# Kernel tuning notes

Measured on AMD Instinct MI355X. Metric: run time of the kernel, lower is better.

Reference implementation:

```python
import jax, jax.numpy as jnp
import numpy as np

SEQ, D = 4096, 1024  # vector_size == dimension == 1024


def setup_inputs() -> dict:
    key = jax.random.key(0)
    ks = jax.random.split(key, 7)
    s = 1.0 / np.sqrt(D)
    return {
        "X": jax.random.normal(ks[0], (SEQ, D), dtype=jnp.float32),
        "Wq": jax.random.normal(ks[1], (D, D), dtype=jnp.float32) * s,
        "bq": jax.random.normal(ks[2], (D,), dtype=jnp.float32) * s,
        "Wk": jax.random.normal(ks[3], (D, D), dtype=jnp.float32) * s,
        "bk": jax.random.normal(ks[4], (D,), dtype=jnp.float32) * s,
        "Wv": jax.random.normal(ks[5], (D, D), dtype=jnp.float32) * s,
        "bv": jax.random.normal(ks[6], (D,), dtype=jnp.float32) * s,
    }


def reference(X, Wq, bq, Wk, bk, Wv, bv):
    # Batched QKV projections (nn.Linear: x @ W^T + b), replacing the per-vector loop.
    Q = X @ Wq.T + bq            # [S, D]
    K = X @ Wk.T + bk            # [S, D]
    V = X @ Wv.T + bv            # [S, D]
    scale = 1.0 / jnp.sqrt(jnp.asarray(D, dtype=X.dtype))
    scores = (Q @ K.T) * scale   # [S, S]
    attn = jax.nn.softmax(scores, axis=1)
    return attn @ V              # [S, D]
```

## Files before the change

kernel.cpp:

```cpp
#include <hip/hip_runtime.h>
#include <hip/hip_bf16.h>
#include <stdint.h>


typedef __bf16 bf16_t;
typedef __bf16 bf16x4 __attribute__((ext_vector_type(4)));
typedef __bf16 bf16x8 __attribute__((ext_vector_type(8)));
typedef float f32x4 __attribute__((ext_vector_type(4)));

#define AS1 __attribute__((address_space(1)))
#define AS3 __attribute__((address_space(3)))

__device__ __forceinline__ void async_ld16(const void* g, void* l) {
  __builtin_amdgcn_global_load_lds((AS1 void*)g, (AS3 void*)l, 16, 0, 0);
}

template <int MODE, int BN, int BK>
__global__ __launch_bounds__(256, 2) void gemm_k(
    const bf16_t* __restrict__ A, const bf16_t* __restrict__ B, const int ld,
    const int Klen,
    bf16_t* __restrict__ o0, bf16_t* __restrict__ o1, bf16_t* __restrict__ o2,
    const float* __restrict__ b0, const float* __restrict__ b1,
    const float* __restrict__ b2, float* __restrict__ fout,
    float* __restrict__ rowsum) {
  constexpr int NF = BN / 32;
  constexpr int KS = BK / 32;
  constexpr int CH = BK / 8;
  constexpr int RS = 256 / CH;
  __shared__ bf16_t As[128 * BK];
  __shared__ bf16_t Bs[BN * BK];

  const int t = threadIdx.x;
  const int lane = t & 63;
  const int wave = t >> 6;
  const int wm = wave >> 1;
  const int wn = wave & 1;
  const int q = lane >> 4;
  const int l16 = lane & 15;
  const int wnoff = wn * (BN / 2);

  int m0, n0;
  if constexpr (MODE == 1) {
    const int bid = blockIdx.y * 32 + blockIdx.x;
    const int xcd = bid & 7, sl = bid >> 3;
    m0 = ((xcd >> 2) * 16 + (sl >> 3)) * 128;
    n0 = ((xcd & 3) * 8 + (sl & 7)) * BN;
  } else {
    n0 = blockIdx.x * BN;
    m0 = blockIdx.y * 128;
  }
  const int k0 = blockIdx.z * Klen;

  const f32x4 zero4 = {0.f, 0.f, 0.f, 0.f};
  f32x4 acc[4][NF];
#pragma unroll
  for (int i = 0; i < 4; ++i)
#pragma unroll
    for (int j = 0; j < NF; ++j) acc[i][j] = zero4;

  const int srow = t / CH;
  const int schunk =
      (t % CH) ^ ((BK == 32) ? ((srow >> 1) & 3) : (srow & 7));
  const bf16_t* Ab = A + (size_t)(m0 + srow) * ld + k0 + schunk * 8;
  const bf16_t* Bb = B + (size_t)(n0 + srow) * ld + k0 + schunk * 8;
  bf16_t* Asl = As + t * 8;
  bf16_t* Bsl = Bs + t * 8;

  const int xf = (BK == 32) ? ((l16 >> 1) & 3) : (l16 & 7);
  const int ar = wm * 64 + l16;
  const int br = wnoff + l16;

  for (int kt = 0; kt < Klen; kt += BK) {
#pragma unroll
    for (int rr = 0; rr < 128 / RS; ++rr)
      async_ld16(Ab + kt + (size_t)(rr * RS) * ld, Asl + rr * RS * BK);
#pragma unroll
    for (int rr = 0; rr < BN / RS; ++rr)
      async_ld16(Bb + kt + (size_t)(rr * RS) * ld, Bsl + rr * RS * BK);
    __syncthreads();

#pragma unroll
    for (int s = 0; s < KS; ++s) {
      bf16x8 fa[4], fb[NF];
#pragma unroll
      for (int im = 0; im < 4; ++im)
        fa[im] = *(const bf16x8*)(As + (ar + im * 16) * BK +
                                  (((s * 4 + q) ^ xf) * 8));
#pragma unroll
      for (int j = 0; j < NF; ++j)
        fb[j] = *(const bf16x8*)(Bs + (br + j * 16) * BK +
                                 (((s * 4 + q) ^ xf) * 8));
#pragma unroll
      for (int im = 0; im < 4; ++im)
#pragma unroll
        for (int j = 0; j < NF; ++j)
          acc[im][j] = __builtin_amdgcn_mfma_f32_16x16x32_bf16(
              fa[im], fb[j], acc[im][j], 0, 0, 0);
    }
    __syncthreads();
  }

  const int mBase = m0 + wm * 64 + q * 4;

  if constexpr (MODE == 0) {
    const int sel = n0 >> 10;
    const int nl0 = (n0 & 1023) + wnoff + l16;
    const float* bias = (sel == 0) ? b0 : ((sel == 1) ? b1 : b2);
    const float sc = (sel == 0) ? 0.03125f : 1.0f;
#pragma unroll
    for (int j = 0; j < NF; ++j) {
      const int nl = nl0 + j * 16;
      const float bb = bias[nl];
#pragma unroll
      for (int im = 0; im < 4; ++im) {
        const int mr = mBase + im * 16;
        if (sel < 2) {
          bf16_t* dst = (sel == 0) ? o0 : o1;
#pragma unroll
          for (int r = 0; r < 4; ++r)
            dst[(size_t)(mr + r) * 1024 + nl] =
                (bf16_t)((acc[im][j][r] + bb) * sc);
        } else {
          bf16x4 v;
#pragma unroll
          for (int r = 0; r < 4; ++r) v[r] = (bf16_t)(acc[im][j][r] + bb);
          *(bf16x4*)(o2 + (size_t)nl * 4096 + mr) = v;
        }
      }
    }
  } else if constexpr (MODE == 1) {
    float ps[4][4];
#pragma unroll
    for (int im = 0; im < 4; ++im)
#pragma unroll
      for (int r = 0; r < 4; ++r) ps[im][r] = 0.f;
#pragma unroll
    for (int j = 0; j < NF; ++j) {
      const int n = n0 + wnoff + j * 16 + l16;
#pragma unroll
      for (int im = 0; im < 4; ++im) {
        const int mr = mBase + im * 16;
#pragma unroll
        for (int r = 0; r < 4; ++r) {
          const float e = __expf(acc[im][j][r]);
          ps[im][r] += e;
          o0[(size_t)(mr + r) * 4096 + n] = (bf16_t)e;
        }
      }
    }
#pragma unroll
    for (int im = 0; im < 4; ++im)
#pragma unroll
      for (int r = 0; r < 4; ++r) {
        float v = ps[im][r];
        v += __shfl_xor(v, 1);
        v += __shfl_xor(v, 2);
        v += __shfl_xor(v, 4);
        v += __shfl_xor(v, 8);
        ps[im][r] = v;
      }
    if (l16 == 0) {
#pragma unroll
      for (int im = 0; im < 4; ++im)
#pragma unroll
        for (int r = 0; r < 4; ++r)
          atomicAdd(rowsum + mBase + im * 16 + r, ps[im][r]);
    }
  } else {
    const int z = blockIdx.z;
    float inv[4][4];
#pragma unroll
    for (int im = 0; im < 4; ++im)
#pragma unroll
      for (int r = 0; r < 4; ++r)
        inv[im][r] = 1.0f / rowsum[mBase + im * 16 + r];
    if (z < 3) {
      bf16_t* pp = (z == 0) ? o0 : ((z == 1) ? o1 : o2);
#pragma unroll
      for (int im = 0; im < 4; ++im) {
        const int mr = mBase + im * 16;
#pragma unroll
        for (int j = 0; j < NF; ++j) {
          const int n = n0 + wnoff + j * 16 + l16;
#pragma unroll
          for (int r = 0; r < 4; ++r)
            pp[(size_t)(mr + r) * 1024 + n] =
                (bf16_t)(acc[im][j][r] * inv[im][r]);
        }
      }
    } else {
#pragma unroll
      for (int im = 0; im < 4; ++im) {
        const int mr = mBase + im * 16;
#pragma unroll
        for (int j = 0; j < NF; ++j) {
          const int n = n0 + wnoff + j * 16 + l16;
#pragma unroll
          for (int r = 0; r < 4; ++r)
            fout[(size_t)(mr + r) * 1024 + n] = acc[im][j][r] * inv[im][r];
        }
      }
    }
  }
}

__global__ __launch_bounds__(256) void cvt_all(
    const float* __restrict__ X, const float* __restrict__ Wq,
    const float* __restrict__ Wk, const float* __restrict__ Wv,
    bf16_t* __restrict__ Xb, bf16_t* __restrict__ Wb,
    float* __restrict__ rowsum) {
  int i = blockIdx.x * 256 + threadIdx.x;
  if (i >= 1835008) {
    rowsum[i - 1835008] = 0.f;
    return;
  }
  const float* src;
  bf16_t* dst;
  int off;
  if (i < 1048576) {
    src = X; dst = Xb; off = i;
  } else {
    const int w = i - 1048576;
    const int sel = w >> 18;
    off = w & 0x3FFFF;
    src = (sel == 0) ? Wq : ((sel == 1) ? Wk : Wv);
    dst = Wb + (size_t)sel * (1024 * 1024);
  }
  const float4 v = ((const float4*)src)[off];
  bf16x4 o;
  o[0] = (bf16_t)v.x; o[1] = (bf16_t)v.y; o[2] = (bf16_t)v.z; o[3] = (bf16_t)v.w;
  ((bf16x4*)dst)[off] = o;
}

__global__ __launch_bounds__(256) void reduce_out(
    const bf16_t* __restrict__ p0, const bf16_t* __restrict__ p1,
    const bf16_t* __restrict__ p2, float* __restrict__ out) {
  const int i = blockIdx.x * 256 + threadIdx.x;
  const bf16x8 a = ((const bf16x8*)p0)[i];
  const bf16x8 b = ((const bf16x8*)p1)[i];
  const bf16x8 c = ((const bf16x8*)p2)[i];
  float4 lo = ((const float4*)out)[2 * i];
  float4 hi = ((const float4*)out)[2 * i + 1];
  lo.x += (float)a[0] + (float)b[0] + (float)c[0];
  lo.y += (float)a[1] + (float)b[1] + (float)c[1];
  lo.z += (float)a[2] + (float)b[2] + (float)c[2];
  lo.w += (float)a[3] + (float)b[3] + (float)c[3];
  hi.x += (float)a[4] + (float)b[4] + (float)c[4];
  hi.y += (float)a[5] + (float)b[5] + (float)c[5];
  hi.z += (float)a[6] + (float)b[6] + (float)c[6];
  hi.w += (float)a[7] + (float)b[7] + (float)c[7];
  ((float4*)out)[2 * i] = lo;
  ((float4*)out)[2 * i + 1] = hi;
}

extern "C" void kernel_launch(void* const* d_in, const int* in_sizes, int n_in,
                              void* d_out, int out_size, void* d_ws,
                              size_t ws_size, hipStream_t stream) {
  const int S = 4096, D = 1024;
  const float* X  = (const float*)d_in[0];
  const float* Wq = (const float*)d_in[1];
  const float* bq = (const float*)d_in[2];
  const float* Wk = (const float*)d_in[3];
  const float* bk = (const float*)d_in[4];
  const float* Wv = (const float*)d_in[5];
  const float* bv = (const float*)d_in[6];
  float* out = (float*)d_out;

  bf16_t* Xb = (bf16_t*)d_ws;
  bf16_t* Wb = Xb + (size_t)S * D;
  bf16_t* Qb = Wb + (size_t)3 * D * D;
  bf16_t* Kb = Qb + (size_t)S * D;
  bf16_t* Vt = Kb + (size_t)S * D;
  bf16_t* Sc = Vt + (size_t)D * S;
  float* rowsum = (float*)(Sc + (size_t)S * S);

  cvt_all<<<7184, 256, 0, stream>>>(X, Wq, Wk, Wv, Xb, Wb, rowsum);

  gemm_k<0, 128, 64><<<dim3(3 * D / 128, S / 128), 256, 0, stream>>>(
      Xb, Wb, D, D, Qb, Kb, Vt, bq, bk, bv, nullptr, nullptr);
  gemm_k<1, 128, 64><<<dim3(S / 128, S / 128), 256, 0, stream>>>(
      Qb, Kb, D, D, Sc, nullptr, nullptr, nullptr, nullptr, nullptr, nullptr,
      rowsum);
  gemm_k<2, 128, 64><<<dim3(D / 128, S / 128, 4), 256, 0, stream>>>(
      Sc, Vt, S, S / 4, Xb, Qb, Kb, nullptr, nullptr, nullptr, out, rowsum);
  reduce_out<<<S * D / 8 / 256, 256, 0, stream>>>(Xb, Qb, Kb, out);
}
```

Measured before the change: 221.4 us.

## Fuse split-K reduction into PV GEMM via last-arriver counter and XCD remap

Removes the separate reduce_out kernel by having each of the four split-K blocks for an output tile increment a per-tile atomic counter. The last arriving block sums the three bf16 partials into the fp32 output. The PV grid is also flattened to 1D with an XCD-aware mapping, so the split-K slices and tiles are spread across dies. The per-tile counters are zeroed by extending cvt_all by one block. This adds threadfences and a serialized tail in the last block of each tile.

Result: slower. 457.0 us (+106.4%).

```diff
diff --git a/kernel.cpp b/kernel.cpp
--- a/kernel.cpp
+++ b/kernel.cpp
@@ -22,7 +22,7 @@
     bf16_t* __restrict__ o0, bf16_t* __restrict__ o1, bf16_t* __restrict__ o2,
     const float* __restrict__ b0, const float* __restrict__ b1,
     const float* __restrict__ b2, float* __restrict__ fout,
-    float* __restrict__ rowsum) {
+    float* __restrict__ rowsum, int* __restrict__ cnt) {
   constexpr int NF = BN / 32;
   constexpr int KS = BK / 32;
   constexpr int CH = BK / 8;
@@ -39,17 +39,29 @@
   const int l16 = lane & 15;
   const int wnoff = wn * (BN / 2);
 
-  int m0, n0;
+  int m0, n0, k0, zz = 0, tileId = 0;
   if constexpr (MODE == 1) {
     const int bid = blockIdx.y * 32 + blockIdx.x;
     const int xcd = bid & 7, sl = bid >> 3;
     m0 = ((xcd >> 2) * 16 + (sl >> 3)) * 128;
     n0 = ((xcd & 3) * 8 + (sl & 7)) * BN;
+    k0 = 0;
+  } else if constexpr (MODE == 2) {
+    const int lin = blockIdx.x;
+    const int xcd = lin & 7;
+    const int s = lin >> 3;
+    zz = xcd >> 1;
+    const int mt = (xcd & 1) * 16 + (s >> 3);
+    const int nt = s & 7;
+    m0 = mt * 128;
+    n0 = nt * 128;
+    k0 = zz * Klen;
+    tileId = mt * 8 + nt;
   } else {
     n0 = blockIdx.x * BN;
     m0 = blockIdx.y * 128;
-  }
-  const int k0 = blockIdx.z * Klen;
+    k0 = blockIdx.z * Klen;
+  }
 
   const f32x4 zero4 = {0.f, 0.f, 0.f, 0.f};
   f32x4 acc[4][NF];
@@ -167,15 +179,14 @@
           atomicAdd(rowsum + mBase + im * 16 + r, ps[im][r]);
     }
   } else {
-    const int z = blockIdx.z;
     float inv[4][4];
 #pragma unroll
     for (int im = 0; im < 4; ++im)
 #pragma unroll
       for (int r = 0; r < 4; ++r)
         inv[im][r] = 1.0f / rowsum[mBase + im * 16 + r];
-    if (z < 3) {
-      bf16_t* pp = (z == 0) ? o0 : ((z == 1) ? o1 : o2);
+    if (zz < 3) {
+      bf16_t* pp = (zz == 0) ? o0 : ((zz == 1) ? o1 : o2);
 #pragma unroll
       for (int im = 0; im < 4; ++im) {
         const int mr = mBase + im * 16;
@@ -199,6 +210,35 @@
           for (int r = 0; r < 4; ++r)
             fout[(size_t)(mr + r) * 1024 + n] = acc[im][j][r] * inv[im][r];
         }
+      }
+    }
+    __threadfence();
+    __syncthreads();
+    __shared__ int lastFlag;
+    if (t == 0) lastFlag = (atomicAdd(cnt + tileId, 1) == 3) ? 1 : 0;
+    __syncthreads();
+    if (lastFlag) {
+      __threadfence();
+      const int rr2 = t >> 1, cb = (t & 1) * 64;
+      const size_t base = (size_t)(m0 + rr2) * 1024 + n0 + cb;
+#pragma unroll
+      for (int kk = 0; kk < 8; ++kk) {
+        const size_t idx = base + kk * 8;
+        const bf16x8 a = *(const bf16x8*)(o0 + idx);
+        const bf16x8 b = *(const bf16x8*)(o1 + idx);
+        const bf16x8 c = *(const bf16x8*)(o2 + idx);
+        float4 lo = *(const float4*)(fout + idx);
+        float4 hi = *(const float4*)(fout + idx + 4);
+        lo.x += (float)a[0] + (float)b[0] + (float)c[0];
+        lo.y += (float)a[1] + (float)b[1] + (float)c[1];
+        lo.z += (float)a[2] + (float)b[2] + (float)c[2];
+        lo.w += (float)a[3] + (float)b[3] + (float)c[3];
+        hi.x += (float)a[4] + (float)b[4] + (float)c[4];
+        hi.y += (float)a[5] + (float)b[5] + (float)c[5];
+        hi.z += (float)a[6] + (float)b[6] + (float)c[6];
+        hi.w += (float)a[7] + (float)b[7] + (float)c[7];
+        *(float4*)(fout + idx) = lo;
+        *(float4*)(fout + idx + 4) = hi;
       }
     }
   }
@@ -230,27 +270,6 @@
   bf16x4 o;
   o[0] = (bf16_t)v.x; o[1] = (bf16_t)v.y; o[2] = (bf16_t)v.z; o[3] = (bf16_t)v.w;
   ((bf16x4*)dst)[off] = o;
-}
-
-__global__ __launch_bounds__(256) void reduce_out(
-    const bf16_t* __restrict__ p0, const bf16_t* __restrict__ p1,
-    const bf16_t* __restrict__ p2, float* __restrict__ out) {
-  const int i = blockIdx.x * 256 + threadIdx.x;
-  const bf16x8 a = ((const bf16x8*)p0)[i];
-  const bf16x8 b = ((const bf16x8*)p1)[i];
-  const bf16x8 c = ((const bf16x8*)p2)[i];
-  float4 lo = ((const float4*)out)[2 * i];
-  float4 hi = ((const float4*)out)[2 * i + 1];
-  lo.x += (float)a[0] + (float)b[0] + (float)c[0];
-  lo.y += (float)a[1] + (float)b[1] + (float)c[1];
-  lo.z += (float)a[2] + (float)b[2] + (float)c[2];
-  lo.w += (float)a[3] + (float)b[3] + (float)c[3];
-  hi.x += (float)a[4] + (float)b[4] + (float)c[4];
-  hi.y += (float)a[5] + (float)b[5] + (float)c[5];
-  hi.z += (float)a[6] + (float)b[6] + (float)c[6];
-  hi.w += (float)a[7] + (float)b[7] + (float)c[7];
-  ((float4*)out)[2 * i] = lo;
-  ((float4*)out)[2 * i + 1] = hi;
 }
 
 extern "C" void kernel_launch(void* const* d_in, const int* in_sizes, int n_in,
@@ -273,15 +292,16 @@
   bf16_t* Vt = Kb + (size_t)S * D;
   bf16_t* Sc = Vt + (size_t)D * S;
   float* rowsum = (float*)(Sc + (size_t)S * S);
-
-  cvt_all<<<7184, 256, 0, stream>>>(X, Wq, Wk, Wv, Xb, Wb, rowsum);
+  int* cnt = (int*)(rowsum + S);
+
+  cvt_all<<<7185, 256, 0, stream>>>(X, Wq, Wk, Wv, Xb, Wb, rowsum);
 
   gemm_k<0, 128, 64><<<dim3(3 * D / 128, S / 128), 256, 0, stream>>>(
-      Xb, Wb, D, D, Qb, Kb, Vt, bq, bk, bv, nullptr, nullptr);
+      Xb, Wb, D, D, Qb, Kb, Vt, bq, bk, bv, nullptr, nullptr, nullptr);
   gemm_k<1, 128, 64><<<dim3(S / 128, S / 128), 256, 0, stream>>>(
       Qb, Kb, D, D, Sc, nullptr, nullptr, nullptr, nullptr, nullptr, nullptr,
-      rowsum);
-  gemm_k<2, 128, 64><<<dim3(D / 128, S / 128, 4), 256, 0, stream>>>(
-      Sc, Vt, S, S / 4, Xb, Qb, Kb, nullptr, nullptr, nullptr, out, rowsum);
-  reduce_out<<<S * D / 8 / 256, 256, 0, stream>>>(Xb, Qb, Kb, out);
+      rowsum, nullptr);
+  gemm_k<2, 128, 64><<<1024, 256, 0, stream>>>(
+      Sc, Vt, S, S / 4, Xb, Qb, Kb, nullptr, nullptr, nullptr, out, rowsum,
+      cnt);
 }
```
